# Kernel optimization log

Measured on AMD Instinct MI355X. Metric: run time of the kernel, lower is better.

The kernel has to match this reference:

```python
import jax, jax.numpy as jnp
import numpy as np
from jax import lax
import math

B, C, H, W = 2, 128, 128, 256
K = 3
KK = K * K
AUX = C + 5

def conv2d(x, w, b, pad):
    out = lax.conv_general_dilated(x, w, (1, 1), [(pad, pad), (pad, pad)],
                                   dimension_numbers=('NCHW', 'OIHW', 'NCHW'))
    return out + b[None, :, None, None]

def erp_coord(h, w):
    xs = jnp.linspace(-math.pi, math.pi, w)
    ys = jnp.linspace(-math.pi / 2, math.pi / 2, h)
    theta = jnp.broadcast_to(xs[None, :], (h, w))
    phi = jnp.broadcast_to(ys[:, None], (h, w))
    return jnp.stack([jnp.sin(theta), jnp.cos(theta), jnp.sin(phi), jnp.cos(phi)], 0)[None]

def freq_energy(x, h, w):
    mag = jnp.abs(jnp.fft.rfft2(x, norm='ortho')).mean(1, keepdims=True)
    # bilinear resize (align_corners=False, half-pixel) to (h, w)
    return jax.image.resize(mag, (x.shape[0], 1, h, w), method='linear', antialias=False)

def deform_sample(x, offset):
    # x: (b,c,H,W); offset: (b, 2*KK, H, W)
    b, c, h, w = x.shape
    off = offset.reshape(b, KK, 2, h, w)
    xx = jnp.arange(w, dtype=x.dtype)[None, None, None, :]
    yy = jnp.arange(h, dtype=x.dtype)[None, None, :, None]
    # align_corners=True normalize/unnormalize cancels exactly
    px = xx + off[:, :, 0]  # (b,KK,h,w)
    py = yy + off[:, :, 1]
    x0 = jnp.floor(px).astype(jnp.int32); x1 = x0 + 1
    y0 = jnp.floor(py).astype(jnp.int32); y1 = y0 + 1
    wx1 = px - x0.astype(x.dtype); wx0 = 1.0 - wx1
    wy1 = py - y0.astype(x.dtype); wy0 = 1.0 - wy1
    flat = x.reshape(b, c, h * w)

    def gather(ix, iy):
        valid = ((ix >= 0) & (ix < w) & (iy >= 0) & (iy < h)).astype(x.dtype)
        idx = jnp.clip(iy, 0, h - 1) * w + jnp.clip(ix, 0, w - 1)  # (b,KK,h,w)
        g = jax.vmap(lambda f, i: f[:, i])(flat, idx)  # (b,c,KK,h,w)
        return g * valid[:, None]

    out = (gather(x0, y0) * (wx0 * wy0)[:, None]
           + gather(x1, y0) * (wx1 * wy0)[:, None]
           + gather(x0, y1) * (wx0 * wy1)[:, None]
           + gather(x1, y1) * (wx1 * wy1)[:, None])
    return out.reshape(b, c * KK, h, w)

def setup_inputs() -> dict:
    key = jax.random.key(0)
    ks = jax.random.split(key, 12)
    s = lambda *sh: 1.0 / np.sqrt(np.prod(sh[1:]))
    def unif(k, *sh):
        return jax.random.uniform(k, sh, jnp.float32, -s(*sh), s(*sh))
    return {
        'x': jax.random.normal(ks[0], (B, C, H, W), jnp.float32),
        'offset_w': unif(ks[1], 2 * KK, AUX, 3, 3),
        'offset_b': jnp.zeros((2 * KK,), jnp.float32),
        'gate_w1': unif(ks[2], AUX // 2, AUX, 3, 3),
        'gate_b1': jnp.zeros((AUX // 2,), jnp.float32),
        'gate_w2': unif(ks[3], 1, AUX // 2, 1, 1),
        'gate_b2': jnp.zeros((1,), jnp.float32),
        'base_w': unif(ks[4], C, C, K, K),
        'base_b': jnp.zeros((C,), jnp.float32),
        'def_w': jax.random.normal(ks[5], (C, C, K, K), jnp.float32) * s(C, C, K, K),
        'def_b': jnp.zeros((C,), jnp.float32),
    }

def reference(x, offset_w, offset_b, gate_w1, gate_b1, gate_w2, gate_b2,
              base_w, base_b, def_w, def_b):
    b, c, h, w = x.shape
    coord = jnp.broadcast_to(erp_coord(h, w), (b, 4, h, w)).astype(x.dtype)
    fe = freq_energy(x, h, w)
    aux = jnp.concatenate([x, coord, fe], 1)
    offset = conv2d(aux, offset_w, offset_b, 1)
    g = jax.nn.relu(conv2d(aux, gate_w1, gate_b1, 1))
    gate = jax.nn.sigmoid(conv2d(g, gate_w2, gate_b2, 0))
    y_base = conv2d(x, base_w, base_b, K // 2)
    sampled = deform_sample(x, offset)  # (b, c*KK, h, w)
    y_def = conv2d(sampled, def_w.reshape(c, c * KK, 1, 1), def_b, 0)
    return (1.0 - gate) * y_base + gate * y_def
```

## Files before the change

### kernel.cpp

```cpp
#include <hip/hip_runtime.h>
#include <hip/hip_bf16.h>

#define BB 2
#define CC 128
#define HH 128
#define WW 256
#define HWs (HH*WW)
#define PI_F 3.14159265358979323846f

typedef __attribute__((ext_vector_type(8))) short bf16x8;
typedef __attribute__((ext_vector_type(8))) unsigned short u16x8;
typedef __attribute__((ext_vector_type(4))) float f32x4;
typedef __attribute__((ext_vector_type(2))) float f32x2;

__device__ __forceinline__ ushort f2bf(float f) {
  uint u = __float_as_uint(f);
  u = (u + 0x7fffu + ((u >> 16) & 1u)) >> 16;
  return (ushort)u;
}
__device__ __forceinline__ float bf2f(ushort u) {
  return __uint_as_float(((uint)u) << 16);
}
__device__ __forceinline__ uint comb4(uint u0, uint u1, uint u2, uint u3,
                                      f32x2 g0, f32x2 g1, f32x2 g2, f32x2 g3) {
  f32x2 a0 = (f32x2){__uint_as_float(u0 << 16), __uint_as_float(u0 & 0xffff0000u)};
  f32x2 a1 = (f32x2){__uint_as_float(u1 << 16), __uint_as_float(u1 & 0xffff0000u)};
  f32x2 a2 = (f32x2){__uint_as_float(u2 << 16), __uint_as_float(u2 & 0xffff0000u)};
  f32x2 a3 = (f32x2){__uint_as_float(u3 << 16), __uint_as_float(u3 & 0xffff0000u)};
  f32x2 s = a0 * g0 + a1 * g1 + a2 * g2 + a3 * g3;
  uint ua = __float_as_uint(s.x) + 0x8000u;
  uint ub = __float_as_uint(s.y) + 0x8000u;
  return (ua >> 16) | (ub & 0xffff0000u);
}

__global__ __launch_bounds__(256) void pack_all_kernel(
    const float* __restrict__ bw, const float* __restrict__ dw,
    const float* __restrict__ ow, const float* __restrict__ gw,
    ushort* __restrict__ apkF, ushort* __restrict__ apkA,
    ushort* __restrict__ a1, ushort* __restrict__ a2) {
  int bid = blockIdx.x;
  int tid = threadIdx.x;
  if (bid < 144) {
    int gid = bid * 256 + tid;
    int lane = gid & 63;
    int kf = (gid >> 6) & 3;
    int mf = (gid >> 8) & 7;
    int chunk = gid >> 11;
    int part = chunk >= 9;
    int tap = part ? chunk - 9 : chunk;
    int m = mf * 16 + (lane & 15);
    int cb = kf * 32 + ((lane >> 4) << 3);
    const float* src = part ? dw : bw;
    ushort* dst = apkF + (size_t)gid * 8;
#pragma unroll
    for (int j = 0; j < 8; ++j)
      dst[j] = f2bf(src[(size_t)m * 1152 + (size_t)(cb + j) * 9 + tap]);
  } else if (bid < 212) {
    int gid = (bid - 144) * 256 + tid;
    if (gid >= 17280) return;
    int lane = gid & 63;
    int kf = (gid >> 6) % 5;
    int mf = (gid / 320) % 6;
    int tap = gid / 1920;
    int m = mf * 16 + (lane & 15);
    int cb = kf * 32 + ((lane >> 4) << 3);
#pragma unroll
    for (int j = 0; j < 8; ++j) {
      int c = cb + j;
      float v = 0.f;
      if (c < 133) {
        if (m < 18) v = ow[(size_t)m * 1197 + c * 9 + tap];
        else if (m < 84) v = gw[(size_t)(m - 18) * 1197 + c * 9 + tap];
      }
      apkA[(size_t)gid * 8 + j] = f2bf(v);
    }
  } else {
    int gid = (bid - 212) * 256 + tid;
    if (gid < 10240) {
      int lane = gid & 63, kf = (gid >> 6) & 7, mf = gid >> 9;
      int m = mf * 16 + (lane & 15);
      int kk0 = kf * 32 + ((lane >> 4) << 3);
#pragma unroll
      for (int j = 0; j < 8; ++j) {
        int kk = kk0 + j;
        float v = 0.f;
        if (m < 129)      { int tt = (m * kk) & 255;         v =  cosf(tt * (PI_F / 128.f)); }
        else if (m < 258) { int tt = ((m - 129) * kk) & 255; v = -sinf(tt * (PI_F / 128.f)); }
        a1[(size_t)gid * 8 + j] = f2bf(v);
      }
    } else if (gid < 18432) {
      int q = gid - 10240;
      int lane = q & 63, kf = (q >> 6) & 7, mf = q >> 9;
      int m = mf * 16 + (lane & 15);
      int g = m & 127;
      int kk0 = kf * 32 + ((lane >> 4) << 3);
#pragma unroll
      for (int j = 0; j < 8; ++j) {
        int kk = kk0 + j;
        int h2 = kk & 127;
        int tt = (g * h2) & 127;
        float ang = tt * (PI_F / 64.f);
        float v = (m < 128) ? ((kk < 128) ? cosf(ang) : sinf(ang))
                            : ((kk < 128) ? -sinf(ang) : cosf(ang));
        a2[(size_t)q * 8 + j] = f2bf(v);
      }
    }
  }
}

__global__ __launch_bounds__(256) void xt_kernel(const float* __restrict__ x,
    ushort* __restrict__ xt) {
  __shared__ ushort sT[64][128];
  int blk = blockIdx.x;
  int b = blk >> 7, h = blk & 127;
  int t = threadIdx.x;
  const float* xb = x + ((size_t)b * CC * HH + h) * WW;
  ushort* ob = xt + (((size_t)b * HH + h) * WW) * 128;
  for (int wt = 0; wt < 4; ++wt) {
    __syncthreads();
    {
      int w = t & 63;
      int sw = (w & 7) << 3;
#pragma unroll
      for (int it = 0; it < 4; ++it) {
        int oct = (t >> 6) + it * 4;
        u16x8 v;
#pragma unroll
        for (int j = 0; j < 8; ++j)
          v[j] = f2bf(xb[(size_t)(oct * 8 + j) * HWs + wt * 64 + w]);
        *(u16x8*)&sT[w][(oct << 3) ^ sw] = v;
      }
    }
    __syncthreads();
#pragma unroll
    for (int it = 0; it < 4; ++it) {
      int u = t + it * 256;
      int w = u >> 4, oct = u & 15;
      u16x8 v = *(const u16x8*)&sT[w][(oct << 3) ^ ((w & 7) << 3)];
      *(u16x8*)&ob[(size_t)(wt * 64 + w) * 128 + oct * 8] = v;
    }
  }
}

__global__ __launch_bounds__(256) void dft1_kernel(const float* __restrict__ x,
    const ushort* __restrict__ a1pk, ushort* __restrict__ F1) {
  int bc = blockIdx.x;
  int t = threadIdx.x, lane = t & 63, wv = t >> 6;
  int q8 = (lane >> 4) << 3, rq = (lane >> 4) << 2;
  const bf16x8* APK = (const bf16x8*)a1pk;
  ushort* f1b = F1 + (size_t)bc * 36864;
  for (int nh = 0; nh < 2; ++nh) {
    f32x4 acc[5][4];
#pragma unroll
    for (int i = 0; i < 5; ++i)
#pragma unroll
      for (int n = 0; n < 4; ++n) acc[i][n] = (f32x4){0.f, 0.f, 0.f, 0.f};
    for (int kf = 0; kf < 8; ++kf) {
      bf16x8 av[5];
#pragma unroll
      for (int i = 0; i < 5; ++i)
        av[i] = APK[(size_t)((wv * 5 + i) * 8 + kf) * 64 + lane];
#pragma unroll
      for (int n2 = 0; n2 < 4; ++n2) {
        int nf = nh * 4 + n2;
        int hh = nf * 16 + (lane & 15);
        const float* xp = x + (((size_t)bc * HH + hh) << 8) + kf * 32 + q8;
        float4 xa = *(const float4*)xp;
        float4 xb4 = *(const float4*)(xp + 4);
        bf16x8 bv;
        bv[0] = (short)f2bf(xa.x); bv[1] = (short)f2bf(xa.y);
        bv[2] = (short)f2bf(xa.z); bv[3] = (short)f2bf(xa.w);
        bv[4] = (short)f2bf(xb4.x); bv[5] = (short)f2bf(xb4.y);
        bv[6] = (short)f2bf(xb4.z); bv[7] = (short)f2bf(xb4.w);
#pragma unroll
        for (int i = 0; i < 5; ++i)
          acc[i][n2] = __builtin_amdgcn_mfma_f32_16x16x32_bf16(av[i], bv, acc[i][n2], 0, 0, 0);
      }
    }
#pragma unroll
    for (int n2 = 0; n2 < 4; ++n2) {
      int hh = (nh * 4 + n2) * 16 + (lane & 15);
#pragma unroll
      for (int i = 0; i < 5; ++i) {
#pragma unroll
        for (int r = 0; r < 4; ++r) {
          int m = (wv * 5 + i) * 16 + rq + r;
          if (m < 258) {
            int sel = m >= 129;
            int k = sel ? m - 129 : m;
            f1b[(size_t)k * 256 + sel * 128 + hh] = f2bf(acc[i][n2][r]);
          }
        }
      }
    }
  }
}

__global__ __launch_bounds__(256) void dft2_kernel(const ushort* __restrict__ F1,
    const ushort* __restrict__ a2pk, float* __restrict__ magbuf) {
  int bc = blockIdx.x;
  int t = threadIdx.x, lane = t & 63, wv = t >> 6;
  int q8 = (lane >> 4) << 3, rq = (lane >> 4) << 2;
  const bf16x8* APK = (const bf16x8*)a2pk;
  const ushort* f1b = F1 + (size_t)bc * 36864;
  float* mb = magbuf + (size_t)bc * 18432;
  for (int ng = 0; ng < 3; ++ng) {
    f32x4 acc[4][3];
#pragma unroll
    for (int i = 0; i < 4; ++i)
#pragma unroll
      for (int n = 0; n < 3; ++n) acc[i][n] = (f32x4){0.f, 0.f, 0.f, 0.f};
    for (int kf = 0; kf < 8; ++kf) {
      bf16x8 av[4];
#pragma unroll
      for (int i = 0; i < 4; ++i) {
        int mf = (i < 2) ? (2 * wv + i) : (2 * wv + (i - 2) + 8);
        av[i] = APK[(size_t)(mf * 8 + kf) * 64 + lane];
      }
#pragma unroll
      for (int n2 = 0; n2 < 3; ++n2) {
        int nf = ng * 3 + n2;
        int krow = nf * 16 + (lane & 15);
        bf16x8 bv = *(const bf16x8*)&f1b[(size_t)krow * 256 + kf * 32 + q8];
#pragma unroll
        for (int i = 0; i < 4; ++i)
          acc[i][n2] = __builtin_amdgcn_mfma_f32_16x16x32_bf16(av[i], bv, acc[i][n2], 0, 0, 0);
      }
    }
#pragma unroll
    for (int n2 = 0; n2 < 3; ++n2) {
      int k = (ng * 3 + n2) * 16 + (lane & 15);
      if (k < 129) {
#pragma unroll
        for (int pr = 0; pr < 2; ++pr) {
#pragma unroll
          for (int r = 0; r < 4; ++r) {
            int g = (2 * wv + pr) * 16 + rq + r;
            float vr = acc[pr][n2][r], vi = acc[pr + 2][n2][r];
            mb[(size_t)g * 144 + k] = sqrtf(vr * vr + vi * vi);
          }
        }
      }
    }
  }
}

__global__ __launch_bounds__(256) void fe_reduce_kernel(const float* __restrict__ magbuf,
    float* __restrict__ fe) {
  int i = blockIdx.x * 256 + threadIdx.x;
  if (i >= 36864) return;
  int k = i % 144;
  int gb = i / 144;
  int g = gb & 127, b = gb >> 7;
  if (k >= 129) return;
  const float* mp = magbuf + (size_t)b * 128 * 18432 + (size_t)g * 144 + k;
  float s = 0.f;
  for (int c = 0; c < 128; ++c) s += mp[(size_t)c * 18432];
  fe[((size_t)b * 128 + g) * 129 + k] = s * (1.0f / (181.01933598375618f * 128.0f));
}

__global__ __launch_bounds__(256) void aux_conv_kernel(
    const ushort* __restrict__ xt, const float* __restrict__ fe,
    const ushort* __restrict__ apk,
    const float* __restrict__ offset_b, const float* __restrict__ gate_b1,
    const float* __restrict__ w2, const float* __restrict__ b2,
    float* __restrict__ offs, float* __restrict__ gate) {
  __shared__ ushort Bt[64][168];
  __shared__ float gld[66][64];
  __shared__ float2 thS[66];
  __shared__ float2 phS[3];
  __shared__ float feS[3][66];
  int t = threadIdx.x;
  int bid = blockIdx.x;
  int lin = (bid & 7) * 128 + (bid >> 3);
  int bz = lin >> 9;
  int rest = lin & 511;
  int h = rest >> 2, w0 = (rest & 3) << 6;
  int lane = t & 63, wid = t >> 6;
  int wm = wid >> 1, wn = wid & 1;
  int q8 = (lane >> 4) << 3, rq = (lane >> 4) << 2;

  if (t < 66) {
    float th = -PI_F + (float)(w0 + t - 1) * (2.0f * PI_F / 255.0f);
    thS[t] = make_float2(sinf(th), cosf(th));
  }
  if (t < 3) {
    float ph = -0.5f * PI_F + (float)(h + t - 1) * (PI_F / 127.0f);
    phS[t] = make_float2(sinf(ph), cosf(ph));
  }
  if (t < 198) {
    int gyi = t / 66, gxi = t % 66;
    int gy = h + gyi - 1, gx = w0 + gxi - 1;
    float v = 0.f;
    if (gy >= 0 && gy < HH && gx >= 0 && gx < WW) {
      float sxc = ((float)gx + 0.5f) * (129.0f / 256.0f) - 0.5f;
      float fx = floorf(sxc);
      int x0 = (int)fx;
      float fr = sxc - fx;
      int x1 = min(x0 + 1, 128);
      x0 = max(x0, 0);
      const float* fb = fe + ((size_t)bz * 128 + gy) * 129;
      v = fb[x0] * (1.f - fr) + fb[x1] * fr;
    }
    feS[gyi][gxi] = v;
  }

  f32x4 acc[3][2];
#pragma unroll
  for (int i = 0; i < 3; ++i) {
    acc[i][0] = (f32x4){0.f, 0.f, 0.f, 0.f};
    acc[i][1] = (f32x4){0.f, 0.f, 0.f, 0.f};
  }
  int p0 = wn * 32 + (lane & 15), p1 = p0 + 16;
  const bf16x8* APK = (const bf16x8*)apk;
  const ushort* xtb = xt + (size_t)bz * 4194304;

  for (int tap = 0; tap < 9; ++tap) {
    int ky = tap / 3 - 1, kx = tap % 3 - 1;
    int gy = h + ky;
    __syncthreads();
    for (int u = t; u < 1280; u += 256) {
      int oct = u >> 6, p = u & 63;
      int gx = w0 + p + kx;
      bool okp = (gy >= 0) && (gy < HH) && ((unsigned)gx < 256u);
      u16x8 v = (u16x8){0, 0, 0, 0, 0, 0, 0, 0};
      if (oct < 16) {
        if (okp) v = *(const u16x8*)&xtb[((((size_t)gy << 8) + gx) << 7) + (oct << 3)];
      } else if (oct == 16) {
        if (okp) {
          float2 tc = thS[p + kx + 1];
          float2 pc = phS[ky + 1];
          float fv = feS[ky + 1][p + kx + 1];
          v[0] = f2bf(tc.x); v[1] = f2bf(tc.y);
          v[2] = f2bf(pc.x); v[3] = f2bf(pc.y);
          v[4] = f2bf(fv);
        }
      }
      *(u16x8*)&Bt[p][oct << 3] = v;
    }
    __syncthreads();
    int fb = (tap * 6 + wm * 3) * 5;
#pragma unroll
    for (int kf = 0; kf < 5; ++kf) {
      int ko = kf * 32 + q8;
      bf16x8 b0 = *(const bf16x8*)&Bt[p0][ko];
      bf16x8 b1 = *(const bf16x8*)&Bt[p1][ko];
#pragma unroll
      for (int mfi = 0; mfi < 3; ++mfi) {
        bf16x8 av = APK[(size_t)(fb + mfi * 5 + kf) * 64 + lane];
        acc[mfi][0] = __builtin_amdgcn_mfma_f32_16x16x32_bf16(av, b0, acc[mfi][0], 0, 0, 0);
        acc[mfi][1] = __builtin_amdgcn_mfma_f32_16x16x32_bf16(av, b1, acc[mfi][1], 0, 0, 0);
      }
    }
  }
#pragma unroll
  for (int nf = 0; nf < 2; ++nf) {
    int p = wn * 32 + nf * 16 + (lane & 15);
    int w = w0 + p;
#pragma unroll
    for (int mfi = 0; mfi < 3; ++mfi) {
#pragma unroll
      for (int r = 0; r < 4; ++r) {
        int oc = wm * 48 + mfi * 16 + rq + r;
        float v = acc[mfi][nf][r];
        if (oc < 18) {
          offs[((size_t)bz * 18 + oc) * HWs + h * WW + w] = v + offset_b[oc];
        } else if (oc < 84) {
          gld[oc - 18][p] = fmaxf(v + gate_b1[oc - 18], 0.f);
        }
      }
    }
  }
  __syncthreads();
  if (t < 64) {
    float s = b2[0];
    for (int c = 0; c < 66; ++c) s = fmaf(gld[c][t], w2[c], s);
    gate[(size_t)bz * HWs + h * WW + w0 + t] = 1.f / (1.f + expf(-s));
  }
}

__global__ __launch_bounds__(256) void fused_out_kernel(
    const ushort* __restrict__ xt, const float* __restrict__ offsp,
    const ushort* __restrict__ apk,
    const float* __restrict__ base_b, const float* __restrict__ def_b,
    const float* __restrict__ gate, float* __restrict__ out) {
  __shared__ ushort Win[4 * 68 * 64];
  __shared__ ushort Bt[2][64][64];
  __shared__ float gvS[64];
  __shared__ float bbS[128], bdS[128];
  int t = threadIdx.x;
  int bid = blockIdx.x;
  int lin = (bid & 7) * 128 + (bid >> 3);
  int bz = lin >> 9;
  int rest = lin & 511;
  int h = rest >> 2, w0 = (rest & 3) << 6;
  int lane = t & 63, wv = t >> 6;
  int l15 = lane & 15, lg = lane >> 4;
  int rq = lg << 2;
  const ushort* xtb = xt + (size_t)bz * 4194304;
  const bf16x8* APK = (const bf16x8*)apk;
  const u16x8 zv = (u16x8){0, 0, 0, 0, 0, 0, 0, 0};

  if (t < 64) gvS[t] = gate[(size_t)bz * HWs + h * WW + w0 + t];
  else if (t < 192) {
    int c = t - 64;
    bbS[c] = base_b[c];
    bdS[c] = def_b[c];
  }

  int p = t & 63, o4 = t >> 6;
  int mw = w0 + p;
  float oxr[9], oyr[9];
#pragma unroll
  for (int d = 0; d < 9; ++d) {
    oxr[d] = offsp[((size_t)bz * 18 + 2 * d) * HWs + h * WW + mw];
    oyr[d] = offsp[((size_t)bz * 18 + 2 * d + 1) * HWs + h * WW + mw];
  }

  f32x4 accB[2][4], accD[2][4];
#pragma unroll
  for (int mi = 0; mi < 2; ++mi)
#pragma unroll
    for (int nf = 0; nf < 4; ++nf) {
      accB[mi][nf] = (f32x4){0.f, 0.f, 0.f, 0.f};
      accD[mi][nf] = (f32x4){0.f, 0.f, 0.f, 0.f};
    }

  for (int half = 0; half < 2; ++half) {
#pragma unroll
    for (int it = 0; it < 9; ++it) {
      int u = it * 256 + t;
      if (u < 2176) {
        int s = u & 7;
        int c = (u >> 3) % 68;
        int r = u / 544;
        int gy = h - 1 + r, gx = w0 - 2 + c;
        u16x8 v = zv;
        if ((unsigned)gy < 128u && (unsigned)gx < 256u)
          v = *(const u16x8*)&xtb[((((size_t)gy << 8) + gx) << 7) + (half << 6) + (s << 3)];
        *(u16x8*)&Win[((r * 68 + c) << 6) + ((s ^ (c & 7)) << 3)] = v;
      }
    }
    __syncthreads();

    auto stage = [&](int nb, int d) {
      float px = (float)mw + oxr[d], py = (float)h + oyr[d];
      float fx = floorf(px), fy = floorf(py);
      int x0 = (int)fx, y0 = (int)fy;
      float wx1 = px - fx, wy1 = py - fy;
      float wx0 = 1.f - wx1, wy0 = 1.f - wy1;
      int x1 = x0 + 1, y1 = y0 + 1;
      bool vx0 = (unsigned)x0 < 256u, vx1 = (unsigned)x1 < 256u;
      bool vy0 = (unsigned)y0 < 128u, vy1 = (unsigned)y1 < 128u;
      float g0 = (vx0 && vy0) ? wx0 * wy0 : 0.f;
      float g1 = (vx1 && vy0) ? wx1 * wy0 : 0.f;
      float g2 = (vx0 && vy1) ? wx0 * wy1 : 0.f;
      float g3 = (vx1 && vy1) ? wx1 * wy1 : 0.f;
      f32x2 G0 = (f32x2){g0, g0}, G1 = (f32x2){g1, g1};
      f32x2 G2 = (f32x2){g2, g2}, G3 = (f32x2){g3, g3};
      int cx0 = min(max(x0, 0), 255), cx1 = min(max(x1, 0), 255);
      int cy0 = min(max(y0, 0), 127), cy1 = min(max(y1, 0), 127);
      int rx0 = cx0 - w0 + 2, rx1 = cx1 - w0 + 2;
      int ry0 = cy0 - h + 1,  ry1 = cy1 - h + 1;
      bool i00 = ((unsigned)ry0 < 4u) && ((unsigned)rx0 < 68u);
      bool i01 = ((unsigned)ry0 < 4u) && ((unsigned)rx1 < 68u);
      bool i10 = ((unsigned)ry1 < 4u) && ((unsigned)rx0 < 68u);
      bool i11 = ((unsigned)ry1 < 4u) && ((unsigned)rx1 < 68u);
      int wb0 = ((ry0 * 68 + rx0) << 6) ^ ((rx0 & 7) << 3);
      int wb1 = ((ry0 * 68 + rx1) << 6) ^ ((rx1 & 7) << 3);
      int wb2 = ((ry1 * 68 + rx0) << 6) ^ ((rx0 & 7) << 3);
      int wb3 = ((ry1 * 68 + rx1) << 6) ^ ((rx1 & 7) << 3);
      int gb0 = (((cy0 << 8) + cx0) << 7) + (half << 6);
      int gb1 = (((cy0 << 8) + cx1) << 7) + (half << 6);
      int gb2 = (((cy1 << 8) + cx0) << 7) + (half << 6);
      int gb3 = (((cy1 << 8) + cx1) << 7) + (half << 6);
#pragma unroll
      for (int oo = 0; oo < 2; ++oo) {
        int o = o4 + oo * 4;
        int o8 = o << 3;
        uint4 c0, c1, c2, c3;
        if (i00) c0 = *(const uint4*)&Win[wb0 ^ o8];
        else     c0 = *(const uint4*)&xtb[gb0 + o8];
        if (i01) c1 = *(const uint4*)&Win[wb1 ^ o8];
        else     c1 = *(const uint4*)&xtb[gb1 + o8];
        if (i10) c2 = *(const uint4*)&Win[wb2 ^ o8];
        else     c2 = *(const uint4*)&xtb[gb2 + o8];
        if (i11) c3 = *(const uint4*)&Win[wb3 ^ o8];
        else     c3 = *(const uint4*)&xtb[gb3 + o8];
        uint4 r;
        r.x = comb4(c0.x, c1.x, c2.x, c3.x, G0, G1, G2, G3);
        r.y = comb4(c0.y, c1.y, c2.y, c3.y, G0, G1, G2, G3);
        r.z = comb4(c0.z, c1.z, c2.z, c3.z, G0, G1, G2, G3);
        r.w = comb4(c0.w, c1.w, c2.w, c3.w, G0, G1, G2, G3);
        *(uint4*)&Bt[nb][p][(o ^ (p & 7)) << 3] = r;
      }
    };

    stage(0, 0);
    __syncthreads();

    int buf = 0;
    for (int d = 0; d < 9; ++d) {
      int ky = d / 3 - 1, kx = d % 3 - 1;
      int ryB = ky + 1;
#pragma unroll
      for (int kfi = 0; kfi < 2; ++kfi) {
        int kff = half * 2 + kfi;
        int segk = kfi * 4 + lg;
        bf16x8 aB0 = APK[(size_t)((d * 8 + wv) * 4 + kff) * 64 + lane];
        bf16x8 aB1 = APK[(size_t)((d * 8 + wv + 4) * 4 + kff) * 64 + lane];
        bf16x8 aD0 = APK[(size_t)(((9 + d) * 8 + wv) * 4 + kff) * 64 + lane];
        bf16x8 aD1 = APK[(size_t)(((9 + d) * 8 + wv + 4) * 4 + kff) * 64 + lane];
#pragma unroll
        for (int nf = 0; nf < 4; ++nf) {
          int pix = nf * 16 + l15;
          int cxr = pix + kx + 2;
          bf16x8 bB = *(const bf16x8*)&Win[((ryB * 68 + cxr) << 6) + ((segk ^ (cxr & 7)) << 3)];
          bf16x8 bD = *(const bf16x8*)&Bt[buf][pix][(segk ^ (pix & 7)) << 3];
          accB[0][nf] = __builtin_amdgcn_mfma_f32_16x16x32_bf16(aB0, bB, accB[0][nf], 0, 0, 0);
          accB[1][nf] = __builtin_amdgcn_mfma_f32_16x16x32_bf16(aB1, bB, accB[1][nf], 0, 0, 0);
          accD[0][nf] = __builtin_amdgcn_mfma_f32_16x16x32_bf16(aD0, bD, accD[0][nf], 0, 0, 0);
          accD[1][nf] = __builtin_amdgcn_mfma_f32_16x16x32_bf16(aD1, bD, accD[1][nf], 0, 0, 0);
        }
      }
      if (d < 8) stage(buf ^ 1, d + 1);
      __syncthreads();
      buf ^= 1;
    }
    if (half == 0) __syncthreads();
  }

#pragma unroll
  for (int nf = 0; nf < 4; ++nf) {
    int pix = nf * 16 + l15;
    float gv = gvS[pix], go = 1.f - gv;
    int w = w0 + pix;
#pragma unroll
    for (int mi = 0; mi < 2; ++mi) {
      int mf = wv + mi * 4;
#pragma unroll
      for (int r = 0; r < 4; ++r) {
        int oc = mf * 16 + rq + r;
        out[(((size_t)bz * CC + oc) << 15) + h * WW + w] =
            go * (accB[mi][nf][r] + bbS[oc]) + gv * (accD[mi][nf][r] + bdS[oc]);
      }
    }
  }
}

extern "C" void kernel_launch(void* const* d_in, const int* in_sizes, int n_in,
                              void* d_out, int out_size, void* d_ws, size_t ws_size,
                              hipStream_t stream) {
  const float* x        = (const float*)d_in[0];
  const float* offset_w = (const float*)d_in[1];
  const float* offset_b = (const float*)d_in[2];
  const float* gate_w1  = (const float*)d_in[3];
  const float* gate_b1  = (const float*)d_in[4];
  const float* gate_w2  = (const float*)d_in[5];
  const float* gate_b2  = (const float*)d_in[6];
  const float* base_w   = (const float*)d_in[7];
  const float* base_b   = (const float*)d_in[8];
  const float* def_w    = (const float*)d_in[9];
  const float* def_b    = (const float*)d_in[10];
  float* out = (float*)d_out;
  float* ws  = (float*)d_ws;

  float* offsb   = ws;
  float* gatebuf = offsb + 1179648;
  float* fe      = gatebuf + 65536;
  float* magbuf  = fe + 33024;
  ushort* xt     = (ushort*)(magbuf + 4718592);
  ushort* F1     = xt + 16777216;
  ushort* a1pk   = F1 + 9437184;
  ushort* a2pk   = a1pk + 81920;
  ushort* apkF   = a2pk + 65536;
  ushort* apkA   = apkF + 294912;

  pack_all_kernel<<<284, 256, 0, stream>>>(base_w, def_w, offset_w, gate_w1,
                                           apkF, apkA, a1pk, a2pk);
  xt_kernel<<<256, 256, 0, stream>>>(x, xt);

  dft1_kernel<<<256, 256, 0, stream>>>(x, a1pk, F1);
  dft2_kernel<<<256, 256, 0, stream>>>(F1, a2pk, magbuf);
  fe_reduce_kernel<<<144, 256, 0, stream>>>(magbuf, fe);

  aux_conv_kernel<<<1024, 256, 0, stream>>>(xt, fe, apkA, offset_b, gate_b1,
                                            gate_w2, gate_b2, offsb, gatebuf);

  fused_out_kernel<<<1024, 256, 0, stream>>>(xt, offsb, apkF, base_b, def_b,
                                             gatebuf, out);
}
```

Before: 196.8 us.

## Spread preprocessing, DFT, and reduction kernels over more blocks to fill GPU

```diff
diff --git a/kernel.cpp b/kernel.cpp
--- a/kernel.cpp
+++ b/kernel.cpp
@@ -33,13 +33,45 @@
   return (ua >> 16) | (ub & 0xffff0000u);
 }
 
-__global__ __launch_bounds__(256) void pack_all_kernel(
+__global__ __launch_bounds__(256) void prep_kernel(
     const float* __restrict__ bw, const float* __restrict__ dw,
     const float* __restrict__ ow, const float* __restrict__ gw,
+    const float* __restrict__ x,
     ushort* __restrict__ apkF, ushort* __restrict__ apkA,
-    ushort* __restrict__ a1, ushort* __restrict__ a2) {
+    ushort* __restrict__ a1, ushort* __restrict__ a2,
+    ushort* __restrict__ xt) {
+  __shared__ ushort sT[64][128];
   int bid = blockIdx.x;
   int tid = threadIdx.x;
+  if (bid >= 284) {
+    int blk = bid - 284;
+    int wt = blk & 3, h = (blk >> 2) & 127, b = blk >> 9;
+    int t = tid;
+    const float* xb = x + ((size_t)b * CC * HH + h) * WW;
+    ushort* ob = xt + (((size_t)b * HH + h) * WW) * 128;
+    {
+      int w = t & 63;
+      int sw = (w & 7) << 3;
+#pragma unroll
+      for (int it = 0; it < 4; ++it) {
+        int oct = (t >> 6) + it * 4;
+        u16x8 v;
+#pragma unroll
+        for (int j = 0; j < 8; ++j)
+          v[j] = f2bf(xb[(size_t)(oct * 8 + j) * HWs + wt * 64 + w]);
+        *(u16x8*)&sT[w][(oct << 3) ^ sw] = v;
+      }
+    }
+    __syncthreads();
+#pragma unroll
+    for (int it = 0; it < 4; ++it) {
+      int u = t + it * 256;
+      int w = u >> 4, oct = u & 15;
+      u16x8 v = *(const u16x8*)&sT[w][(oct << 3) ^ ((w & 7) << 3)];
+      *(u16x8*)&ob[(size_t)(wt * 64 + w) * 128 + oct * 8] = v;
+    }
+    return;
+  }
   if (bid < 144) {
     int gid = bid * 256 + tid;
     int lane = gid & 63;
@@ -108,88 +140,53 @@
   }
 }
 
-__global__ __launch_bounds__(256) void xt_kernel(const float* __restrict__ x,
-    ushort* __restrict__ xt) {
-  __shared__ ushort sT[64][128];
-  int blk = blockIdx.x;
-  int b = blk >> 7, h = blk & 127;
-  int t = threadIdx.x;
-  const float* xb = x + ((size_t)b * CC * HH + h) * WW;
-  ushort* ob = xt + (((size_t)b * HH + h) * WW) * 128;
-  for (int wt = 0; wt < 4; ++wt) {
-    __syncthreads();
-    {
-      int w = t & 63;
-      int sw = (w & 7) << 3;
-#pragma unroll
-      for (int it = 0; it < 4; ++it) {
-        int oct = (t >> 6) + it * 4;
-        u16x8 v;
-#pragma unroll
-        for (int j = 0; j < 8; ++j)
-          v[j] = f2bf(xb[(size_t)(oct * 8 + j) * HWs + wt * 64 + w]);
-        *(u16x8*)&sT[w][(oct << 3) ^ sw] = v;
-      }
-    }
-    __syncthreads();
-#pragma unroll
-    for (int it = 0; it < 4; ++it) {
-      int u = t + it * 256;
-      int w = u >> 4, oct = u & 15;
-      u16x8 v = *(const u16x8*)&sT[w][(oct << 3) ^ ((w & 7) << 3)];
-      *(u16x8*)&ob[(size_t)(wt * 64 + w) * 128 + oct * 8] = v;
-    }
-  }
-}
-
 __global__ __launch_bounds__(256) void dft1_kernel(const float* __restrict__ x,
     const ushort* __restrict__ a1pk, ushort* __restrict__ F1) {
-  int bc = blockIdx.x;
+  int bid = blockIdx.x;
+  int bc = bid >> 1, nh = bid & 1;
   int t = threadIdx.x, lane = t & 63, wv = t >> 6;
   int q8 = (lane >> 4) << 3, rq = (lane >> 4) << 2;
   const bf16x8* APK = (const bf16x8*)a1pk;
   ushort* f1b = F1 + (size_t)bc * 36864;
-  for (int nh = 0; nh < 2; ++nh) {
-    f32x4 acc[5][4];
+  f32x4 acc[5][4];
+#pragma unroll
+  for (int i = 0; i < 5; ++i)
+#pragma unroll
+    for (int n = 0; n < 4; ++n) acc[i][n] = (f32x4){0.f, 0.f, 0.f, 0.f};
+  for (int kf = 0; kf < 8; ++kf) {
+    bf16x8 av[5];
 #pragma unroll
     for (int i = 0; i < 5; ++i)
-#pragma unroll
-      for (int n = 0; n < 4; ++n) acc[i][n] = (f32x4){0.f, 0.f, 0.f, 0.f};
-    for (int kf = 0; kf < 8; ++kf) {
-      bf16x8 av[5];
+      av[i] = APK[(size_t)((wv * 5 + i) * 8 + kf) * 64 + lane];
+#pragma unroll
+    for (int n2 = 0; n2 < 4; ++n2) {
+      int nf = nh * 4 + n2;
+      int hh = nf * 16 + (lane & 15);
+      const float* xp = x + (((size_t)bc * HH + hh) << 8) + kf * 32 + q8;
+      float4 xa = *(const float4*)xp;
+      float4 xb4 = *(const float4*)(xp + 4);
+      bf16x8 bv;
+      bv[0] = (short)f2bf(xa.x); bv[1] = (short)f2bf(xa.y);
+      bv[2] = (short)f2bf(xa.z); bv[3] = (short)f2bf(xa.w);
+      bv[4] = (short)f2bf(xb4.x); bv[5] = (short)f2bf(xb4.y);
+      bv[6] = (short)f2bf(xb4.z); bv[7] = (short)f2bf(xb4.w);
 #pragma unroll
       for (int i = 0; i < 5; ++i)
-        av[i] = APK[(size_t)((wv * 5 + i) * 8 + kf) * 64 + lane];
-#pragma unroll
-      for (int n2 = 0; n2 < 4; ++n2) {
-        int nf = nh * 4 + n2;
-        int hh = nf * 16 + (lane & 15);
-        const float* xp = x + (((size_t)bc * HH + hh) << 8) + kf * 32 + q8;
-        float4 xa = *(const float4*)xp;
-        float4 xb4 = *(const float4*)(xp + 4);
-        bf16x8 bv;
-        bv[0] = (short)f2bf(xa.x); bv[1] = (short)f2bf(xa.y);
-        bv[2] = (short)f2bf(xa.z); bv[3] = (short)f2bf(xa.w);
-        bv[4] = (short)f2bf(xb4.x); bv[5] = (short)f2bf(xb4.y);
-        bv[6] = (short)f2bf(xb4.z); bv[7] = (short)f2bf(xb4.w);
-#pragma unroll
-        for (int i = 0; i < 5; ++i)
-          acc[i][n2] = __builtin_amdgcn_mfma_f32_16x16x32_bf16(av[i], bv, acc[i][n2], 0, 0, 0);
-      }
-    }
-#pragma unroll
-    for (int n2 = 0; n2 < 4; ++n2) {
-      int hh = (nh * 4 + n2) * 16 + (lane & 15);
-#pragma unroll
-      for (int i = 0; i < 5; ++i) {
-#pragma unroll
-        for (int r = 0; r < 4; ++r) {
-          int m = (wv * 5 + i) * 16 + rq + r;
-          if (m < 258) {
-            int sel = m >= 129;
-            int k = sel ? m - 129 : m;
-            f1b[(size_t)k * 256 + sel * 128 + hh] = f2bf(acc[i][n2][r]);
-          }
+        acc[i][n2] = __builtin_amdgcn_mfma_f32_16x16x32_bf16(av[i], bv, acc[i][n2], 0, 0, 0);
+    }
+  }
+#pragma unroll
+  for (int n2 = 0; n2 < 4; ++n2) {
+    int hh = (nh * 4 + n2) * 16 + (lane & 15);
+#pragma unroll
+    for (int i = 0; i < 5; ++i) {
+#pragma unroll
+      for (int r = 0; r < 4; ++r) {
+        int m = (wv * 5 + i) * 16 + rq + r;
+        if (m < 258) {
+          int sel = m >= 129;
+          int k = sel ? m - 129 : m;
+          f1b[(size_t)k * 256 + sel * 128 + hh] = f2bf(acc[i][n2][r]);
         }
       }
     }
@@ -198,47 +195,46 @@
 
 __global__ __launch_bounds__(256) void dft2_kernel(const ushort* __restrict__ F1,
     const ushort* __restrict__ a2pk, float* __restrict__ magbuf) {
-  int bc = blockIdx.x;
+  int bid = blockIdx.x;
+  int bc = bid / 3, ng = bid % 3;
   int t = threadIdx.x, lane = t & 63, wv = t >> 6;
   int q8 = (lane >> 4) << 3, rq = (lane >> 4) << 2;
   const bf16x8* APK = (const bf16x8*)a2pk;
   const ushort* f1b = F1 + (size_t)bc * 36864;
   float* mb = magbuf + (size_t)bc * 18432;
-  for (int ng = 0; ng < 3; ++ng) {
-    f32x4 acc[4][3];
-#pragma unroll
-    for (int i = 0; i < 4; ++i)
-#pragma unroll
-      for (int n = 0; n < 3; ++n) acc[i][n] = (f32x4){0.f, 0.f, 0.f, 0.f};
-    for (int kf = 0; kf < 8; ++kf) {
-      bf16x8 av[4];
-#pragma unroll
-      for (int i = 0; i < 4; ++i) {
-        int mf = (i < 2) ? (2 * wv + i) : (2 * wv + (i - 2) + 8);
-        av[i] = APK[(size_t)(mf * 8 + kf) * 64 + lane];
-      }
-#pragma unroll
-      for (int n2 = 0; n2 < 3; ++n2) {
-        int nf = ng * 3 + n2;
-        int krow = nf * 16 + (lane & 15);
-        bf16x8 bv = *(const bf16x8*)&f1b[(size_t)krow * 256 + kf * 32 + q8];
-#pragma unroll
-        for (int i = 0; i < 4; ++i)
-          acc[i][n2] = __builtin_amdgcn_mfma_f32_16x16x32_bf16(av[i], bv, acc[i][n2], 0, 0, 0);
-      }
+  f32x4 acc[4][3];
+#pragma unroll
+  for (int i = 0; i < 4; ++i)
+#pragma unroll
+    for (int n = 0; n < 3; ++n) acc[i][n] = (f32x4){0.f, 0.f, 0.f, 0.f};
+  for (int kf = 0; kf < 8; ++kf) {
+    bf16x8 av[4];
+#pragma unroll
+    for (int i = 0; i < 4; ++i) {
+      int mf = (i < 2) ? (2 * wv + i) : (2 * wv + (i - 2) + 8);
+      av[i] = APK[(size_t)(mf * 8 + kf) * 64 + lane];
     }
 #pragma unroll
     for (int n2 = 0; n2 < 3; ++n2) {
-      int k = (ng * 3 + n2) * 16 + (lane & 15);
-      if (k < 129) {
-#pragma unroll
-        for (int pr = 0; pr < 2; ++pr) {
-#pragma unroll
-          for (int r = 0; r < 4; ++r) {
-            int g = (2 * wv + pr) * 16 + rq + r;
-            float vr = acc[pr][n2][r], vi = acc[pr + 2][n2][r];
-            mb[(size_t)g * 144 + k] = sqrtf(vr * vr + vi * vi);
-          }
+      int nf = ng * 3 + n2;
+      int krow = nf * 16 + (lane & 15);
+      bf16x8 bv = *(const bf16x8*)&f1b[(size_t)krow * 256 + kf * 32 + q8];
+#pragma unroll
+      for (int i = 0; i < 4; ++i)
+        acc[i][n2] = __builtin_amdgcn_mfma_f32_16x16x32_bf16(av[i], bv, acc[i][n2], 0, 0, 0);
+    }
+  }
+#pragma unroll
+  for (int n2 = 0; n2 < 3; ++n2) {
+    int k = (ng * 3 + n2) * 16 + (lane & 15);
+    if (k < 129) {
+#pragma unroll
+      for (int pr = 0; pr < 2; ++pr) {
+#pragma unroll
+        for (int r = 0; r < 4; ++r) {
+          int g = (2 * wv + pr) * 16 + rq + r;
+          float vr = acc[pr][n2][r], vi = acc[pr + 2][n2][r];
+          mb[(size_t)g * 144 + k] = sqrtf(vr * vr + vi * vi);
         }
       }
     }
@@ -247,16 +243,21 @@
 
 __global__ __launch_bounds__(256) void fe_reduce_kernel(const float* __restrict__ magbuf,
     float* __restrict__ fe) {
-  int i = blockIdx.x * 256 + threadIdx.x;
+  int bid = blockIdx.x;
+  int i = (bid >> 3) * 256 + threadIdx.x;
+  int cq = bid & 7;
   if (i >= 36864) return;
   int k = i % 144;
   int gb = i / 144;
   int g = gb & 127, b = gb >> 7;
   if (k >= 129) return;
-  const float* mp = magbuf + (size_t)b * 128 * 18432 + (size_t)g * 144 + k;
+  const float* mp = magbuf + (size_t)b * 128 * 18432 + (size_t)g * 144 + k
+                  + (size_t)cq * 16 * 18432;
   float s = 0.f;
-  for (int c = 0; c < 128; ++c) s += mp[(size_t)c * 18432];
-  fe[((size_t)b * 128 + g) * 129 + k] = s * (1.0f / (181.01933598375618f * 128.0f));
+#pragma unroll
+  for (int c = 0; c < 16; ++c) s += mp[(size_t)c * 18432];
+  atomicAdd(&fe[((size_t)b * 128 + g) * 129 + k],
+            s * (1.0f / (181.01933598375618f * 128.0f)));
 }
 
 __global__ __launch_bounds__(256) void aux_conv_kernel(
@@ -576,13 +577,13 @@
   ushort* apkF   = a2pk + 65536;
   ushort* apkA   = apkF + 294912;
 
-  pack_all_kernel<<<284, 256, 0, stream>>>(base_w, def_w, offset_w, gate_w1,
-                                           apkF, apkA, a1pk, a2pk);
-  xt_kernel<<<256, 256, 0, stream>>>(x, xt);
-
-  dft1_kernel<<<256, 256, 0, stream>>>(x, a1pk, F1);
-  dft2_kernel<<<256, 256, 0, stream>>>(F1, a2pk, magbuf);
-  fe_reduce_kernel<<<144, 256, 0, stream>>>(magbuf, fe);
+  hipMemsetAsync(fe, 0, 33024 * sizeof(float), stream);
+  prep_kernel<<<1308, 256, 0, stream>>>(base_w, def_w, offset_w, gate_w1, x,
+                                        apkF, apkA, a1pk, a2pk, xt);
+
+  dft1_kernel<<<512, 256, 0, stream>>>(x, a1pk, F1);
+  dft2_kernel<<<768, 256, 0, stream>>>(F1, a2pk, magbuf);
+  fe_reduce_kernel<<<1152, 256, 0, stream>>>(magbuf, fe);
 
   aux_conv_kernel<<<1024, 256, 0, stream>>>(xt, fe, apkA, offset_b, gate_b1,
                                             gate_w2, gate_b2, offsb, gatebuf);
```

Result: no change. 197.1 us (+0.2%).
